# Kernel tuning notes

Measured on AMD Instinct MI355X. Metric: run time of the kernel, lower is better.

The kernel has to match this reference:

```python
import jax, jax.numpy as jnp
import numpy as np

NUM_NODES = 100000
NUM_EDGES = 600000
NUM_GRAPHS = 1000
EMB = 128


def setup_inputs() -> dict:
    key = jax.random.key(0)
    ks = jax.random.split(key, 12)
    x = jax.random.normal(ks[0], (NUM_NODES, 4), dtype=jnp.float32)
    edge_index = jax.random.randint(ks[1], (2, NUM_EDGES), 0, NUM_NODES, dtype=jnp.int32)
    x_scalar = jax.random.normal(ks[2], (NUM_GRAPHS, 4), dtype=jnp.float32)
    batch_index = jnp.sort(jax.random.randint(ks[3], (NUM_NODES,), 0, NUM_GRAPHS, dtype=jnp.int32))
    def glorot(k, shape):
        fan_in, fan_out = shape[0], shape[1]
        s = jnp.sqrt(2.0 / (fan_in + fan_out)).astype(jnp.float32)
        return jax.random.normal(k, shape, dtype=jnp.float32) * s
    return {
        "x": x,
        "edge_index": edge_index,
        "x_scalar": x_scalar,
        "batch_index": batch_index,
        "W0": glorot(ks[4], (4, EMB)), "b0": jnp.zeros((EMB,), jnp.float32),
        "W1": glorot(ks[5], (EMB, EMB)), "b1": jnp.zeros((EMB,), jnp.float32),
        "W2": glorot(ks[6], (EMB, EMB)), "b2": jnp.zeros((EMB,), jnp.float32),
        "W3": glorot(ks[7], (EMB, EMB)), "b3": jnp.zeros((EMB,), jnp.float32),
        "Wl1": glorot(ks[8], (EMB + 4, 64)), "bl1": jnp.zeros((64,), jnp.float32),
        "Wl2": glorot(ks[9], (64, 1)), "bl2": jnp.zeros((1,), jnp.float32),
    }


def _gcn_norm(edge_index, num_nodes):
    # PyG GCNConv default: add self-loops, symmetric normalization
    loop = jnp.arange(num_nodes, dtype=edge_index.dtype)
    src = jnp.concatenate([edge_index[0], loop])
    dst = jnp.concatenate([edge_index[1], loop])
    deg = jax.ops.segment_sum(jnp.ones_like(src, dtype=jnp.float32), dst,
                              num_segments=num_nodes)
    dinv = jnp.where(deg > 0, jax.lax.rsqrt(jnp.maximum(deg, 1e-12)), 0.0)
    norm = dinv[src] * dinv[dst]  # [E+N]
    return src, dst, norm


def _gcn_conv(h, src, dst, norm, W, b, num_nodes):
    h = h @ W                                   # [N, out]
    msg = h[src] * norm[:, None]                # gather + normalize
    out = jax.ops.segment_sum(msg, dst, num_segments=num_nodes)  # scatter-add
    return out + b


def reference(x, edge_index, x_scalar, batch_index,
              W0, b0, W1, b1, W2, b2, W3, b3, Wl1, bl1, Wl2, bl2):
    n = x.shape[0]
    src, dst, norm = _gcn_norm(edge_index, n)
    h = jax.nn.relu(_gcn_conv(x, src, dst, norm, W0, b0, n))
    h = jax.nn.relu(_gcn_conv(h, src, dst, norm, W1, b1, n))
    h = jax.nn.relu(_gcn_conv(h, src, dst, norm, W2, b2, n))
    h = jax.nn.relu(_gcn_conv(h, src, dst, norm, W3, b3, n))
    # global mean pool over batch_index
    sums = jax.ops.segment_sum(h, batch_index, num_segments=NUM_GRAPHS)
    cnts = jax.ops.segment_sum(jnp.ones((n,), jnp.float32), batch_index,
                               num_segments=NUM_GRAPHS)
    pooled = sums / jnp.maximum(cnts, 1.0)[:, None]          # [G, EMB]
    feat = jnp.concatenate([pooled, x_scalar], axis=1)       # [G, EMB+4]
    out = jax.nn.relu(feat @ Wl1 + bl1) @ Wl2 + bl2          # [G, 1]
    return out
```

## Files before the change

### kernel.cpp

```cpp
#include <hip/hip_runtime.h>

#define NN 100000
#define EE 600000
#define GG 1000
#define NB ((NN + 255) / 256)
#define CAP 32
#define LDSPAD 136

typedef __bf16 bf16x8 __attribute__((ext_vector_type(8)));
typedef float f32x4 __attribute__((ext_vector_type(4)));
typedef unsigned int u32;

__device__ inline float2 bf2_to_f2(u32 u) {
  return make_float2(__uint_as_float(u << 16), __uint_as_float(u & 0xffff0000u));
}
__device__ inline u32 f2_to_bf2(float a, float b) {
  union { __bf16 h[2]; u32 u; } pk;
  pk.h[0] = (__bf16)a; pk.h[1] = (__bf16)b;
  return pk.u;
}


__global__ void k_init(int* cnt, int* gstart) {
  int i = blockIdx.x * 256 + threadIdx.x;
  if (i < NN) cnt[i] = 0;
  if (i <= GG) gstart[i] = NN;
}

__global__ void k_fill(const int* __restrict__ src, const int* __restrict__ dst,
                       int* cnt, int* __restrict__ ibucket) {
  int e = blockIdx.x * 256 + threadIdx.x;
  if (e >= EE) return;
  int s = src[e], d = dst[e];
  int pos = atomicAdd(&cnt[d], 1);
  if (pos < CAP - 1) ibucket[d * CAP + pos] = s;
}

__global__ void k_prep(const int* __restrict__ cnt, float* __restrict__ dinv,
                       const int* __restrict__ batch, int* gstart,
                       const float* __restrict__ W1, const float* __restrict__ W2,
                       const float* __restrict__ W3,
                       __bf16* __restrict__ Wt1, __bf16* __restrict__ Wt2,
                       __bf16* __restrict__ Wt3) {
  int gid = blockIdx.x * 256 + threadIdx.x;
  if (gid < NN) {
    dinv[gid] = rsqrtf((float)(cnt[gid] + 1));
    int b = batch[gid];
    if (gid == 0) {
      for (int g = 0; g <= b; ++g) gstart[g] = 0;
    } else {
      int prev = batch[gid - 1];
      for (int g = prev + 1; g <= b; ++g) gstart[g] = gid;
    }
  }
  if (gid < 3 * 16384) {
    int which = gid >> 14, idx = gid & 16383;
    int n = idx >> 7, k = idx & 127;
    const float* W = (which == 0) ? W1 : (which == 1) ? W2 : W3;
    __bf16* Wt = (which == 0) ? Wt1 : (which == 1) ? Wt2 : Wt3;
    Wt[(size_t)n * 128 + k] = (__bf16)W[(size_t)k * 128 + n];
  }
}

__global__ void k_wb(const int* __restrict__ ibucket, const int* __restrict__ cnt,
                     const float* __restrict__ dinv, int2* __restrict__ wbucket) {
  int gid = blockIdx.x * 256 + threadIdx.x;
  if (gid >= NN * CAP) return;
  int d = gid >> 5, slot = gid & 31;
  int m = min(cnt[d], CAP - 1);
  int mp = (m + 8) & ~7;
  if (slot >= mp) return;
  float dd = dinv[d];
  int s; float w;
  if (slot < m)      { s = ibucket[gid]; w = dinv[s] * dd; }
  else if (slot == m){ s = d;            w = dd * dd; }
  else               { s = d;            w = 0.f; }
  wbucket[gid] = make_int2(s, __float_as_int(w));
}


__global__ void k_aggx(const float4* __restrict__ x, const int* __restrict__ cnt,
                       const int2* __restrict__ wbucket, float4* __restrict__ y) {
  int i = blockIdx.x * 256 + threadIdx.x;
  if (i >= NN) return;
  int m1 = min(cnt[i], CAP - 1) + 1;
  float4 acc = make_float4(0.f, 0.f, 0.f, 0.f);
  for (int e = 0; e < m1; ++e) {
    int2 md = wbucket[i * CAP + e];
    float w = __int_as_float(md.y);
    float4 v = x[md.x];
    acc.x = fmaf(w, v.x, acc.x);
    acc.y = fmaf(w, v.y, acc.y);
    acc.z = fmaf(w, v.z, acc.z);
    acc.w = fmaf(w, v.w, acc.w);
  }
  y[i] = acc;
}


__global__ void k_lin0(const float4* __restrict__ y, const float* __restrict__ W0,
                       const float* __restrict__ b0, u32* __restrict__ hout2) {
  int gid = blockIdx.x * 256 + threadIdx.x;
  if (gid >= NN * 16) return;
  int node = gid >> 4, cg = gid & 15;
  float4 yv = y[node];
  float v[8];
  #pragma unroll
  for (int k = 0; k < 2; ++k) {
    float4 b = *(const float4*)(b0 + cg * 8 + k * 4);
    v[k * 4 + 0] = b.x; v[k * 4 + 1] = b.y; v[k * 4 + 2] = b.z; v[k * 4 + 3] = b.w;
  }
  #pragma unroll
  for (int k = 0; k < 4; ++k) {
    float yk = (k == 0) ? yv.x : (k == 1) ? yv.y : (k == 2) ? yv.z : yv.w;
    float4 wa = *(const float4*)(W0 + k * 128 + cg * 8);
    float4 wb = *(const float4*)(W0 + k * 128 + cg * 8 + 4);
    v[0] = fmaf(yk, wa.x, v[0]); v[1] = fmaf(yk, wa.y, v[1]);
    v[2] = fmaf(yk, wa.z, v[2]); v[3] = fmaf(yk, wa.w, v[3]);
    v[4] = fmaf(yk, wb.x, v[4]); v[5] = fmaf(yk, wb.y, v[5]);
    v[6] = fmaf(yk, wb.z, v[6]); v[7] = fmaf(yk, wb.w, v[7]);
  }
  uint4 o;
  o.x = f2_to_bf2(fmaxf(v[0], 0.f), fmaxf(v[1], 0.f));
  o.y = f2_to_bf2(fmaxf(v[2], 0.f), fmaxf(v[3], 0.f));
  o.z = f2_to_bf2(fmaxf(v[4], 0.f), fmaxf(v[5], 0.f));
  o.w = f2_to_bf2(fmaxf(v[6], 0.f), fmaxf(v[7], 0.f));
  *(uint4*)(hout2 + (size_t)node * 64 + cg * 4) = o;
}

__global__ __launch_bounds__(256) void k_agg23(const __bf16* __restrict__ hlin,
                                               const int* __restrict__ cnt,
                                               const int2* __restrict__ wbucket,
                                               u32* __restrict__ hout2) {
  int node = blockIdx.x * 4 + (threadIdx.x >> 6);
  int lane = threadIdx.x & 63;
  int ln = lane & 15, quad = lane >> 4;
  if (node >= NN) return;
  int mp = (min(cnt[node], CAP - 1) + 8) & ~7;
  int2 me = wbucket[(size_t)node * CAP + (lane & 31)];
  int s_l = me.x, w_l = me.y;

  float acc[8] = {0.f, 0.f, 0.f, 0.f, 0.f, 0.f, 0.f, 0.f};
  for (int j = 0; j < mp; j += 8) {
    int p0 = (j + quad) * 4, p1 = (j + 4 + quad) * 4;
    int se0 = __builtin_amdgcn_ds_bpermute(p0, s_l);
    int se1 = __builtin_amdgcn_ds_bpermute(p1, s_l);
    float w0e = __int_as_float(__builtin_amdgcn_ds_bpermute(p0, w_l));
    float w1e = __int_as_float(__builtin_amdgcn_ds_bpermute(p1, w_l));
    uint4 u0 = *(const uint4*)(hlin + ((size_t)se0 << 7) + ln * 8);
    uint4 u1 = *(const uint4*)(hlin + ((size_t)se1 << 7) + ln * 8);
    float2 f;
    f = bf2_to_f2(u0.x); acc[0] = fmaf(w0e, f.x, acc[0]); acc[1] = fmaf(w0e, f.y, acc[1]);
    f = bf2_to_f2(u0.y); acc[2] = fmaf(w0e, f.x, acc[2]); acc[3] = fmaf(w0e, f.y, acc[3]);
    f = bf2_to_f2(u0.z); acc[4] = fmaf(w0e, f.x, acc[4]); acc[5] = fmaf(w0e, f.y, acc[5]);
    f = bf2_to_f2(u0.w); acc[6] = fmaf(w0e, f.x, acc[6]); acc[7] = fmaf(w0e, f.y, acc[7]);
    f = bf2_to_f2(u1.x); acc[0] = fmaf(w1e, f.x, acc[0]); acc[1] = fmaf(w1e, f.y, acc[1]);
    f = bf2_to_f2(u1.y); acc[2] = fmaf(w1e, f.x, acc[2]); acc[3] = fmaf(w1e, f.y, acc[3]);
    f = bf2_to_f2(u1.z); acc[4] = fmaf(w1e, f.x, acc[4]); acc[5] = fmaf(w1e, f.y, acc[5]);
    f = bf2_to_f2(u1.w); acc[6] = fmaf(w1e, f.x, acc[6]); acc[7] = fmaf(w1e, f.y, acc[7]);
  }
  #pragma unroll
  for (int k = 0; k < 8; ++k) {
    acc[k] += __shfl_xor(acc[k], 16);
    acc[k] += __shfl_xor(acc[k], 32);
  }
  if (quad == 0) {
    uint4 o;
    o.x = f2_to_bf2(acc[0], acc[1]);
    o.y = f2_to_bf2(acc[2], acc[3]);
    o.z = f2_to_bf2(acc[4], acc[5]);
    o.w = f2_to_bf2(acc[6], acc[7]);
    *(uint4*)(hout2 + (size_t)node * 64 + ln * 4) = o;
  }
}

__global__ __launch_bounds__(256) void k_mfma(const __bf16* __restrict__ hin,
                                              const __bf16* __restrict__ Wt,
                                              const float* __restrict__ bias,
                                              __bf16* __restrict__ hout) {
  __shared__ __bf16 As[128 * LDSPAD];
  int tid = threadIdx.x;
  int row0 = blockIdx.x * 128;
  int lane = tid & 63, w = tid >> 6;
  int ln = lane & 15, quad = lane >> 4;

  bf16x8 bfrag[8][4];
  float bcol[8];
  #pragma unroll
  for (int nt = 0; nt < 8; ++nt) {
    bcol[nt] = bias[nt * 16 + ln];
    #pragma unroll
    for (int kc = 0; kc < 4; ++kc)
      bfrag[nt][kc] = *(const bf16x8*)(Wt + (size_t)(nt * 16 + ln) * 128 + kc * 32 + quad * 8);
  }

  #pragma unroll
  for (int i = 0; i < 8; ++i) {
    int eb = (i * 256 + tid) * 8;
    int r = eb >> 7, c = eb & 127;
    int gr = row0 + r;
    uint4 v = make_uint4(0, 0, 0, 0);
    if (gr < NN) v = *(const uint4*)(hin + (size_t)gr * 128 + c);
    *(uint4*)&As[r * LDSPAD + c] = v;
  }
  __syncthreads();

  f32x4 acc[2][8];
  #pragma unroll
  for (int rt = 0; rt < 2; ++rt)
    #pragma unroll
    for (int nt = 0; nt < 8; ++nt) acc[rt][nt] = (f32x4){0.f, 0.f, 0.f, 0.f};

  #pragma unroll
  for (int kc = 0; kc < 4; ++kc) {
    bf16x8 a0 = *(const bf16x8*)&As[(w * 32 + ln) * LDSPAD + kc * 32 + quad * 8];
    bf16x8 a1 = *(const bf16x8*)&As[(w * 32 + 16 + ln) * LDSPAD + kc * 32 + quad * 8];
    #pragma unroll
    for (int nt = 0; nt < 8; ++nt) {
      acc[0][nt] = __builtin_amdgcn_mfma_f32_16x16x32_bf16(a0, bfrag[nt][kc], acc[0][nt], 0, 0, 0);
      acc[1][nt] = __builtin_amdgcn_mfma_f32_16x16x32_bf16(a1, bfrag[nt][kc], acc[1][nt], 0, 0, 0);
    }
  }

  #pragma unroll
  for (int rt = 0; rt < 2; ++rt)
    #pragma unroll
    for (int nt = 0; nt < 8; ++nt)
      #pragma unroll
      for (int reg = 0; reg < 4; ++reg) {
        int gr = row0 + w * 32 + rt * 16 + quad * 4 + reg;
        if (gr < NN)
          hout[(size_t)gr * 128 + nt * 16 + ln] =
              (__bf16)fmaxf(acc[rt][nt][reg] + bcol[nt], 0.f);
      }
}

__global__ __launch_bounds__(256) void k_poolmlp(const uint2* __restrict__ h4u,
                                                 const int* __restrict__ gstart,
                                                 const float* __restrict__ xs,
                                                 const float* __restrict__ Wl1,
                                                 const float* __restrict__ bl1,
                                                 const float* __restrict__ Wl2,
                                                 const float* __restrict__ bl2,
                                                 float* __restrict__ out) {
  __shared__ float4 part[8][32];
  __shared__ float pooled[128];
  int g = blockIdx.x;
  int beg = gstart[g], end = gstart[g + 1];
  int tid = threadIdx.x;
  int cg = tid & 31;
  int rg = tid >> 5;
  float4 acc = make_float4(0.f, 0.f, 0.f, 0.f);
  for (int i = beg + rg; i < end; i += 8) {
    uint2 u = h4u[(size_t)i * 32 + cg];
    acc.x += __uint_as_float(u.x << 16);
    acc.y += __uint_as_float(u.x & 0xffff0000u);
    acc.z += __uint_as_float(u.y << 16);
    acc.w += __uint_as_float(u.y & 0xffff0000u);
  }
  part[rg][cg] = acc;
  __syncthreads();
  if (tid < 32) {
    float4 s = part[0][tid];
    #pragma unroll
    for (int r = 1; r < 8; ++r) {
      float4 v = part[r][tid];
      s.x += v.x; s.y += v.y; s.z += v.z; s.w += v.w;
    }
    float sc = 1.f / fmaxf((float)(end - beg), 1.f);
    pooled[tid * 4 + 0] = s.x * sc;
    pooled[tid * 4 + 1] = s.y * sc;
    pooled[tid * 4 + 2] = s.z * sc;
    pooled[tid * 4 + 3] = s.w * sc;
  }
  __syncthreads();
  if (tid < 64) {
    float hj = bl1[tid];
    #pragma unroll 4
    for (int k = 0; k < 128; ++k) hj = fmaf(pooled[k], Wl1[k * 64 + tid], hj);
    const float* xr = xs + g * 4;
    #pragma unroll
    for (int k = 0; k < 4; ++k) hj = fmaf(xr[k], Wl1[(128 + k) * 64 + tid], hj);
    hj = fmaxf(hj, 0.f);
    float val = hj * Wl2[tid];
    #pragma unroll
    for (int off = 32; off > 0; off >>= 1) val += __shfl_down(val, off);
    if (tid == 0) out[g] = val + bl2[0];
  }
}


extern "C" void kernel_launch(void* const* d_in, const int* in_sizes, int n_in,
                              void* d_out, int out_size, void* d_ws, size_t ws_size,
                              hipStream_t stream) {
  const float* x    = (const float*)d_in[0];
  const int*   ei   = (const int*)d_in[1];
  const float* xs   = (const float*)d_in[2];
  const int*   batch= (const int*)d_in[3];
  const float* W0   = (const float*)d_in[4];
  const float* b0   = (const float*)d_in[5];
  const float* W1   = (const float*)d_in[6];
  const float* b1   = (const float*)d_in[7];
  const float* W2   = (const float*)d_in[8];
  const float* b2   = (const float*)d_in[9];
  const float* W3   = (const float*)d_in[10];
  const float* b3   = (const float*)d_in[11];
  const float* Wl1  = (const float*)d_in[12];
  const float* bl1  = (const float*)d_in[13];
  const float* Wl2  = (const float*)d_in[14];
  const float* bl2  = (const float*)d_in[15];
  const int* srcA = ei;
  const int* dstA = ei + EE;
  float* out = (float*)d_out;

  char* p = (char*)d_ws;
  auto take = [&](size_t bytes) { char* q = p; p += (bytes + 255) & ~(size_t)255; return q; };
  __bf16* hA    = (__bf16*)take((size_t)NN * 128 * 2);
  __bf16* hB    = (__bf16*)take((size_t)NN * 128 * 2);
  float*  y     = (float*)take((size_t)NN * 4 * 4);
  int*    cnt   = (int*)take((size_t)NN * 4);
  float*  dinv  = (float*)take((size_t)NN * 4);
  int*    ibucket = (int*)take((size_t)NN * CAP * 4);
  int2*   wbucket = (int2*)take((size_t)NN * CAP * 8);
  int*    gstart= (int*)take((size_t)(GG + 1) * 4);
  __bf16* Wt1   = (__bf16*)take(16384 * 2);
  __bf16* Wt2   = (__bf16*)take(16384 * 2);
  __bf16* Wt3   = (__bf16*)take(16384 * 2);

  k_init<<<NB, 256, 0, stream>>>(cnt, gstart);
  k_fill<<<(EE + 255) / 256, 256, 0, stream>>>(srcA, dstA, cnt, ibucket);
  k_prep<<<NB, 256, 0, stream>>>(cnt, dinv, batch, gstart, W1, W2, W3, Wt1, Wt2, Wt3);
  k_wb<<<(NN * CAP + 255) / 256, 256, 0, stream>>>(ibucket, cnt, dinv, wbucket);

  k_aggx<<<NB, 256, 0, stream>>>((const float4*)x, cnt, wbucket, (float4*)y);
  k_lin0<<<(NN * 16 + 255) / 256, 256, 0, stream>>>((const float4*)y, W0, b0, (u32*)hA);
  k_agg23<<<(NN + 3) / 4, 256, 0, stream>>>(hA, cnt, wbucket, (u32*)hB);
  k_mfma<<<(NN + 127) / 128, 256, 0, stream>>>(hB, Wt1, b1, hA);
  k_agg23<<<(NN + 3) / 4, 256, 0, stream>>>(hA, cnt, wbucket, (u32*)hB);
  k_mfma<<<(NN + 127) / 128, 256, 0, stream>>>(hB, Wt2, b2, hA);
  k_agg23<<<(NN + 3) / 4, 256, 0, stream>>>(hA, cnt, wbucket, (u32*)hB);
  k_mfma<<<(NN + 127) / 128, 256, 0, stream>>>(hB, Wt3, b3, hA);

  k_poolmlp<<<GG, 256, 0, stream>>>((const uint2*)hA, gstart, xs, Wl1, bl1, Wl2, bl2, out);
}
```

Measured before the change: 355.1 us.

## Fuse neighbor aggregation into MFMA linear kernel via LDS staging

Merges the per-node gather/aggregate kernel with the following MFMA dense layer. Each wave aggregates its 32 rows (two nodes per iteration, one per half-wave) and writes them straight into the LDS A tile, so the intermediate bf16 buffer is no longer written to and re-read from global memory. W fragments are now loaded inside the MFMA loop rather than preloaded into registers, which saves registers. The trade-off is lower parallelism per node: 128 nodes per block processed serially in 16 steps, with load imbalance between the two paired nodes.

```diff
diff --git a/kernel.cpp b/kernel.cpp
--- a/kernel.cpp
+++ b/kernel.cpp
@@ -128,82 +128,80 @@
   *(uint4*)(hout2 + (size_t)node * 64 + cg * 4) = o;
 }
 
-__global__ __launch_bounds__(256) void k_agg23(const __bf16* __restrict__ hlin,
+
+__device__ __forceinline__ void gather8(const __bf16* __restrict__ hlin, int j,
+                                        int quad, int ln, int s_l, int w_l,
+                                        int srcoff, float acc[8]) {
+  int p0 = srcoff + (j + quad) * 4;
+  int p1 = srcoff + (j + 4 + quad) * 4;
+  int se0 = __builtin_amdgcn_ds_bpermute(p0, s_l);
+  int se1 = __builtin_amdgcn_ds_bpermute(p1, s_l);
+  float w0e = __int_as_float(__builtin_amdgcn_ds_bpermute(p0, w_l));
+  float w1e = __int_as_float(__builtin_amdgcn_ds_bpermute(p1, w_l));
+  uint4 u0 = *(const uint4*)(hlin + ((size_t)se0 << 7) + ln * 8);
+  uint4 u1 = *(const uint4*)(hlin + ((size_t)se1 << 7) + ln * 8);
+  float2 f;
+  f = bf2_to_f2(u0.x); acc[0] = fmaf(w0e, f.x, acc[0]); acc[1] = fmaf(w0e, f.y, acc[1]);
+  f = bf2_to_f2(u0.y); acc[2] = fmaf(w0e, f.x, acc[2]); acc[3] = fmaf(w0e, f.y, acc[3]);
+  f = bf2_to_f2(u0.z); acc[4] = fmaf(w0e, f.x, acc[4]); acc[5] = fmaf(w0e, f.y, acc[5]);
+  f = bf2_to_f2(u0.w); acc[6] = fmaf(w0e, f.x, acc[6]); acc[7] = fmaf(w0e, f.y, acc[7]);
+  f = bf2_to_f2(u1.x); acc[0] = fmaf(w1e, f.x, acc[0]); acc[1] = fmaf(w1e, f.y, acc[1]);
+  f = bf2_to_f2(u1.y); acc[2] = fmaf(w1e, f.x, acc[2]); acc[3] = fmaf(w1e, f.y, acc[3]);
+  f = bf2_to_f2(u1.z); acc[4] = fmaf(w1e, f.x, acc[4]); acc[5] = fmaf(w1e, f.y, acc[5]);
+  f = bf2_to_f2(u1.w); acc[6] = fmaf(w1e, f.x, acc[6]); acc[7] = fmaf(w1e, f.y, acc[7]);
+}
+
+__global__ __launch_bounds__(256) void k_aggmm(const __bf16* __restrict__ hin,
                                                const int* __restrict__ cnt,
                                                const int2* __restrict__ wbucket,
-                                               u32* __restrict__ hout2) {
-  int node = blockIdx.x * 4 + (threadIdx.x >> 6);
-  int lane = threadIdx.x & 63;
-  int ln = lane & 15, quad = lane >> 4;
-  if (node >= NN) return;
-  int mp = (min(cnt[node], CAP - 1) + 8) & ~7;
-  int2 me = wbucket[(size_t)node * CAP + (lane & 31)];
-  int s_l = me.x, w_l = me.y;
-
-  float acc[8] = {0.f, 0.f, 0.f, 0.f, 0.f, 0.f, 0.f, 0.f};
-  for (int j = 0; j < mp; j += 8) {
-    int p0 = (j + quad) * 4, p1 = (j + 4 + quad) * 4;
-    int se0 = __builtin_amdgcn_ds_bpermute(p0, s_l);
-    int se1 = __builtin_amdgcn_ds_bpermute(p1, s_l);
-    float w0e = __int_as_float(__builtin_amdgcn_ds_bpermute(p0, w_l));
-    float w1e = __int_as_float(__builtin_amdgcn_ds_bpermute(p1, w_l));
-    uint4 u0 = *(const uint4*)(hlin + ((size_t)se0 << 7) + ln * 8);
-    uint4 u1 = *(const uint4*)(hlin + ((size_t)se1 << 7) + ln * 8);
-    float2 f;
-    f = bf2_to_f2(u0.x); acc[0] = fmaf(w0e, f.x, acc[0]); acc[1] = fmaf(w0e, f.y, acc[1]);
-    f = bf2_to_f2(u0.y); acc[2] = fmaf(w0e, f.x, acc[2]); acc[3] = fmaf(w0e, f.y, acc[3]);
-    f = bf2_to_f2(u0.z); acc[4] = fmaf(w0e, f.x, acc[4]); acc[5] = fmaf(w0e, f.y, acc[5]);
-    f = bf2_to_f2(u0.w); acc[6] = fmaf(w0e, f.x, acc[6]); acc[7] = fmaf(w0e, f.y, acc[7]);
-    f = bf2_to_f2(u1.x); acc[0] = fmaf(w1e, f.x, acc[0]); acc[1] = fmaf(w1e, f.y, acc[1]);
-    f = bf2_to_f2(u1.y); acc[2] = fmaf(w1e, f.x, acc[2]); acc[3] = fmaf(w1e, f.y, acc[3]);
-    f = bf2_to_f2(u1.z); acc[4] = fmaf(w1e, f.x, acc[4]); acc[5] = fmaf(w1e, f.y, acc[5]);
-    f = bf2_to_f2(u1.w); acc[6] = fmaf(w1e, f.x, acc[6]); acc[7] = fmaf(w1e, f.y, acc[7]);
-  }
-  #pragma unroll
-  for (int k = 0; k < 8; ++k) {
-    acc[k] += __shfl_xor(acc[k], 16);
-    acc[k] += __shfl_xor(acc[k], 32);
-  }
-  if (quad == 0) {
-    uint4 o;
-    o.x = f2_to_bf2(acc[0], acc[1]);
-    o.y = f2_to_bf2(acc[2], acc[3]);
-    o.z = f2_to_bf2(acc[4], acc[5]);
-    o.w = f2_to_bf2(acc[6], acc[7]);
-    *(uint4*)(hout2 + (size_t)node * 64 + ln * 4) = o;
-  }
-}
-
-__global__ __launch_bounds__(256) void k_mfma(const __bf16* __restrict__ hin,
-                                              const __bf16* __restrict__ Wt,
-                                              const float* __restrict__ bias,
-                                              __bf16* __restrict__ hout) {
+                                               const __bf16* __restrict__ Wt,
+                                               const float* __restrict__ bias,
+                                               __bf16* __restrict__ hout) {
   __shared__ __bf16 As[128 * LDSPAD];
   int tid = threadIdx.x;
   int row0 = blockIdx.x * 128;
   int lane = tid & 63, w = tid >> 6;
   int ln = lane & 15, quad = lane >> 4;
-
-  bf16x8 bfrag[8][4];
+  int wbase = row0 + w * 32;
+
+  for (int t = 0; t < 16; ++t) {
+    int na = wbase + t, nb = wbase + 16 + t;
+    int nodeL = (lane < 32) ? na : nb;
+    int2 me = make_int2(0, 0);
+    if (nodeL < NN) me = wbucket[(size_t)nodeL * CAP + (lane & 31)];
+    int s_l = me.x, w_l = me.y;
+    int mpa = (na < NN) ? ((min(cnt[na], CAP - 1) + 8) & ~7) : 0;
+    int mpb = (nb < NN) ? ((min(cnt[nb], CAP - 1) + 8) & ~7) : 0;
+    float aa[8] = {0.f, 0.f, 0.f, 0.f, 0.f, 0.f, 0.f, 0.f};
+    float ab[8] = {0.f, 0.f, 0.f, 0.f, 0.f, 0.f, 0.f, 0.f};
+    int mpmin = min(mpa, mpb);
+    int j = 0;
+    for (; j < mpmin; j += 8) {
+      gather8(hin, j, quad, ln, s_l, w_l, 0, aa);
+      gather8(hin, j, quad, ln, s_l, w_l, 128, ab);
+    }
+    for (; j < mpa; j += 8) gather8(hin, j, quad, ln, s_l, w_l, 0, aa);
+    for (; j < mpb; j += 8) gather8(hin, j, quad, ln, s_l, w_l, 128, ab);
+    #pragma unroll
+    for (int k = 0; k < 8; ++k) {
+      aa[k] += __shfl_xor(aa[k], 16); aa[k] += __shfl_xor(aa[k], 32);
+      ab[k] += __shfl_xor(ab[k], 16); ab[k] += __shfl_xor(ab[k], 32);
+    }
+    if (quad == 0) {
+      uint4 oa, ob;
+      oa.x = f2_to_bf2(aa[0], aa[1]); oa.y = f2_to_bf2(aa[2], aa[3]);
+      oa.z = f2_to_bf2(aa[4], aa[5]); oa.w = f2_to_bf2(aa[6], aa[7]);
+      ob.x = f2_to_bf2(ab[0], ab[1]); ob.y = f2_to_bf2(ab[2], ab[3]);
+      ob.z = f2_to_bf2(ab[4], ab[5]); ob.w = f2_to_bf2(ab[6], ab[7]);
+      *(uint4*)&As[(w * 32 + t) * LDSPAD + ln * 8] = oa;
+      *(uint4*)&As[(w * 32 + 16 + t) * LDSPAD + ln * 8] = ob;
+    }
+  }
+  __syncthreads();
+
   float bcol[8];
   #pragma unroll
-  for (int nt = 0; nt < 8; ++nt) {
-    bcol[nt] = bias[nt * 16 + ln];
-    #pragma unroll
-    for (int kc = 0; kc < 4; ++kc)
-      bfrag[nt][kc] = *(const bf16x8*)(Wt + (size_t)(nt * 16 + ln) * 128 + kc * 32 + quad * 8);
-  }
-
-  #pragma unroll
-  for (int i = 0; i < 8; ++i) {
-    int eb = (i * 256 + tid) * 8;
-    int r = eb >> 7, c = eb & 127;
-    int gr = row0 + r;
-    uint4 v = make_uint4(0, 0, 0, 0);
-    if (gr < NN) v = *(const uint4*)(hin + (size_t)gr * 128 + c);
-    *(uint4*)&As[r * LDSPAD + c] = v;
-  }
-  __syncthreads();
+  for (int nt = 0; nt < 8; ++nt) bcol[nt] = bias[nt * 16 + ln];
 
   f32x4 acc[2][8];
   #pragma unroll
@@ -217,8 +215,9 @@
     bf16x8 a1 = *(const bf16x8*)&As[(w * 32 + 16 + ln) * LDSPAD + kc * 32 + quad * 8];
     #pragma unroll
     for (int nt = 0; nt < 8; ++nt) {
-      acc[0][nt] = __builtin_amdgcn_mfma_f32_16x16x32_bf16(a0, bfrag[nt][kc], acc[0][nt], 0, 0, 0);
-      acc[1][nt] = __builtin_amdgcn_mfma_f32_16x16x32_bf16(a1, bfrag[nt][kc], acc[1][nt], 0, 0, 0);
+      bf16x8 bf = *(const bf16x8*)(Wt + (size_t)(nt * 16 + ln) * 128 + kc * 32 + quad * 8);
+      acc[0][nt] = __builtin_amdgcn_mfma_f32_16x16x32_bf16(a0, bf, acc[0][nt], 0, 0, 0);
+      acc[1][nt] = __builtin_amdgcn_mfma_f32_16x16x32_bf16(a1, bf, acc[1][nt], 0, 0, 0);
     }
   }
 
@@ -334,12 +333,9 @@
 
   k_aggx<<<NB, 256, 0, stream>>>((const float4*)x, cnt, wbucket, (float4*)y);
   k_lin0<<<(NN * 16 + 255) / 256, 256, 0, stream>>>((const float4*)y, W0, b0, (u32*)hA);
-  k_agg23<<<(NN + 3) / 4, 256, 0, stream>>>(hA, cnt, wbucket, (u32*)hB);
-  k_mfma<<<(NN + 127) / 128, 256, 0, stream>>>(hB, Wt1, b1, hA);
-  k_agg23<<<(NN + 3) / 4, 256, 0, stream>>>(hA, cnt, wbucket, (u32*)hB);
-  k_mfma<<<(NN + 127) / 128, 256, 0, stream>>>(hB, Wt2, b2, hA);
-  k_agg23<<<(NN + 3) / 4, 256, 0, stream>>>(hA, cnt, wbucket, (u32*)hB);
-  k_mfma<<<(NN + 127) / 128, 256, 0, stream>>>(hB, Wt3, b3, hA);
-
-  k_poolmlp<<<GG, 256, 0, stream>>>((const uint2*)hA, gstart, xs, Wl1, bl1, Wl2, bl2, out);
-}
+  k_aggmm<<<(NN + 127) / 128, 256, 0, stream>>>(hA, cnt, wbucket, Wt1, b1, hB);
+  k_aggmm<<<(NN + 127) / 128, 256, 0, stream>>>(hB, cnt, wbucket, Wt2, b2, hA);
+  k_aggmm<<<(NN + 127) / 128, 256, 0, stream>>>(hA, cnt, wbucket, Wt3, b3, hB);
+
+  k_poolmlp<<<GG, 256, 0, stream>>>((const uint2*)hB, gstart, xs, Wl1, bl1, Wl2, bl2, out);
+}
```

Result: slower. 415.3 us (+17.0%).
